# Kernel optimization log

Hardware: AMD Instinct MI355X
Metric: run time of the kernel (lower is better)

Reference implementation:

```python
import jax, jax.numpy as jnp
import numpy as np

NUM_CLASSES = 81
THRESHOLD = 0.5
NEGPOS_RATIO = 3
VARIANCE = (0.1, 0.2)


def point_form(p):
    # center-size -> corner form
    return jnp.concatenate([p[:, :2] - p[:, 2:] / 2, p[:, :2] + p[:, 2:] / 2], axis=1)


def jaccard(box_a, box_b):
    # box_a: [O,4] corners, box_b: [P,4] corners -> IoU [O,P]
    lt = jnp.maximum(box_a[:, None, :2], box_b[None, :, :2])
    rb = jnp.minimum(box_a[:, None, 2:], box_b[None, :, 2:])
    wh = jnp.clip(rb - lt, 0.0)
    inter = wh[..., 0] * wh[..., 1]
    area_a = ((box_a[:, 2] - box_a[:, 0]) * (box_a[:, 3] - box_a[:, 1]))[:, None]
    area_b = ((box_b[:, 2] - box_b[:, 0]) * (box_b[:, 3] - box_b[:, 1]))[None, :]
    return inter / (area_a + area_b - inter)


def encode(matched, priors, variances):
    # matched: [P,4] corner GT, priors: [P,4] center-size
    g_cxcy = (matched[:, :2] + matched[:, 2:]) / 2 - priors[:, :2]
    g_cxcy = g_cxcy / (variances[0] * priors[:, 2:])
    g_wh = (matched[:, 2:] - matched[:, :2]) / priors[:, 2:]
    g_wh = jnp.log(g_wh) / variances[1]
    return jnp.concatenate([g_cxcy, g_wh], axis=1)


def match_one(truths, labels, priors):
    overlaps = jaccard(truths, point_form(priors))   # [O,P]
    best_prior_idx = jnp.argmax(overlaps, axis=1)     # [O] best prior per truth
    best_truth_overlap = jnp.max(overlaps, axis=0)    # [P]
    best_truth_idx = jnp.argmax(overlaps, axis=0)     # [P] best truth per prior
    # force each truth's best prior to match that truth
    best_truth_overlap = best_truth_overlap.at[best_prior_idx].set(2.0)
    best_truth_idx = best_truth_idx.at[best_prior_idx].set(jnp.arange(truths.shape[0]))
    matched = truths[best_truth_idx]                  # [P,4]
    conf = labels[best_truth_idx].astype(jnp.int32) + 1
    conf = jnp.where(best_truth_overlap < THRESHOLD, 0, conf)
    loc = encode(matched, priors, VARIANCE)
    return loc, conf


def _loss(loc_data, conf_data, targets, priors):
    B, P, C = conf_data.shape
    loc_t, conf_t = jax.vmap(lambda t: match_one(t[:, :4], t[:, 4], priors))(targets)
    pos = conf_t > 0                                  # [B,P]
    # smooth-L1 (beta=1) over positive priors, sum reduction
    d = loc_data - loc_t
    sl1 = jnp.where(jnp.abs(d) < 1.0, 0.5 * d * d, jnp.abs(d) - 0.5)
    loss_l = jnp.sum(jnp.where(pos[..., None], sl1, 0.0))
    # per-prior CE used both for mining ranking and the final conf loss
    ce = jax.nn.logsumexp(conf_data, axis=-1) - jnp.take_along_axis(
        conf_data, conf_t[..., None], axis=-1)[..., 0]   # [B,P]
    # hard negative mining: zero positives, double argsort for rank
    loss_c_rank = jnp.where(pos, 0.0, ce)
    loss_idx = jnp.argsort(-loss_c_rank, axis=1)
    idx_rank = jnp.argsort(loss_idx, axis=1)
    num_pos = jnp.sum(pos, axis=1, keepdims=True)     # [B,1]
    num_neg = jnp.minimum(NEGPOS_RATIO * num_pos, P - 1)
    neg = idx_rank < num_neg
    sel = pos | neg
    loss_c = jnp.sum(jnp.where(sel, ce, 0.0))
    N = jnp.sum(num_pos).astype(loc_data.dtype)
    return loss_l / N, loss_c / N


def setup_inputs():
    key = jax.random.key(0)
    kl, kc, kb1, kb2, kll, kp1, kp2 = jax.random.split(key, 7)
    B, P, O, C = 64, 8732, 50, NUM_CLASSES
    loc_data = jax.random.normal(kl, (B, P, 4), jnp.float32)
    conf_data = jax.random.normal(kc, (B, P, C), jnp.float32)
    # valid GT boxes in corner form inside [0,1]
    cxcy = jax.random.uniform(kb1, (B, O, 2), minval=0.2, maxval=0.8)
    wh = jax.random.uniform(kb2, (B, O, 2), minval=0.05, maxval=0.3)
    boxes = jnp.concatenate([cxcy - wh / 2, cxcy + wh / 2], axis=-1)
    labels = jax.random.randint(kll, (B, O), 0, C - 1).astype(jnp.float32)
    targets = jnp.concatenate([boxes, labels[..., None]], axis=-1)  # [B,O,5]
    # priors in center-size form
    pcxcy = jax.random.uniform(kp1, (P, 2), minval=0.05, maxval=0.95)
    pwh = jax.random.uniform(kp2, (P, 2), minval=0.05, maxval=0.5)
    priors = jnp.concatenate([pcxcy, pwh], axis=-1)
    return {"loc_data": loc_data, "conf_data": conf_data, "targets": targets, "priors": priors}


def reference(loc_data, conf_data, targets, priors):
    return _loss(loc_data, conf_data, targets, priors)
```

## Files before the change

### kernel.cpp

```cpp
#include <hip/hip_runtime.h>
#include <float.h>

#pragma clang fp contract(off)

typedef unsigned long long ull;
typedef unsigned int u32;

#define THRESH 0.5f
#define PPT 4
#define CE_R 128
#define SEL_T 512
#define ENC_SEG 1024


__device__ __forceinline__ float sl1(float d) {
    float a = fabsf(d);
    return (a < 1.f) ? 0.5f * d * d : a - 0.5f;
}

__global__ __launch_bounds__(256) void k_match(
        const float* __restrict__ targets, const float* __restrict__ priors,
        float* __restrict__ bto, int* __restrict__ bti, int P, int O, int SEG) {
    const int b = blockIdx.y, seg = blockIdx.x;
    __shared__ float4 tbox[128];
    __shared__ float tarea[128];
    const float* trow = targets + (size_t)b * O * 5;
    for (int o = threadIdx.x; o < O; o += blockDim.x) {
        float x1 = trow[o * 5 + 0], y1 = trow[o * 5 + 1];
        float x2 = trow[o * 5 + 2], y2 = trow[o * 5 + 3];
        tbox[o] = make_float4(x1, y1, x2, y2);
        tarea[o] = (x2 - x1) * (y2 - y1);
    }
    __syncthreads();
    const int p0 = seg * SEG;
    float px1[PPT], py1[PPT], px2[PPT], py2[PPT], pa[PPT];
    float bestv[PPT]; int besto[PPT]; int pidx[PPT];
#pragma unroll
    for (int j = 0; j < PPT; j++) {
        int p = p0 + (int)threadIdx.x + j * 256;
        pidx[j] = p; bestv[j] = -1.f; besto[j] = 0;
        if (p < P) {
            float4 pr = ((const float4*)priors)[p];
            px1[j] = pr.x - pr.z / 2.f;
            py1[j] = pr.y - pr.w / 2.f;
            px2[j] = pr.x + pr.z / 2.f;
            py2[j] = pr.y + pr.w / 2.f;
            pa[j] = (px2[j] - px1[j]) * (py2[j] - py1[j]);
        } else {
            px1[j] = 2.f; py1[j] = 2.f; px2[j] = 2.f; py2[j] = 2.f; pa[j] = 1.f;
        }
    }
    for (int o = 0; o < O; o++) {
        float4 t = tbox[o];
        float ta = tarea[o];
#pragma unroll
        for (int j = 0; j < PPT; j++) {
            float lx = fmaxf(t.x, px1[j]), ly = fmaxf(t.y, py1[j]);
            float rx = fminf(t.z, px2[j]), ry = fminf(t.w, py2[j]);
            float wx = fmaxf(rx - lx, 0.f), wy = fmaxf(ry - ly, 0.f);
            float inter = wx * wy;
            float iou = 0.f;
            if (inter > 0.f) iou = inter / (ta + pa[j] - inter);
            if (iou > bestv[j]) { bestv[j] = iou; besto[j] = o; }
        }
    }
#pragma unroll
    for (int j = 0; j < PPT; j++) {
        if (pidx[j] < P) {
            bto[(size_t)b * P + pidx[j]] = bestv[j];
            bti[(size_t)b * P + pidx[j]] = besto[j];
        }
    }
}

__global__ __launch_bounds__(256) void k_tbest(
        const float* __restrict__ targets, const float* __restrict__ priors,
        ull* __restrict__ tbest, int P, int O, int npairs) {
    int g = blockIdx.x * 4 + ((int)threadIdx.x >> 6);
    int lane = threadIdx.x & 63;
    if (g >= npairs) return;
    int OP = (O + 1) >> 1;
    int b = g / OP;
    int o0 = (g % OP) * 2;
    const float* trow = targets + ((size_t)b * O + o0) * 5;
    float ax1 = trow[0], ay1 = trow[1], ax2 = trow[2], ay2 = trow[3];
    float ta0 = (ax2 - ax1) * (ay2 - ay1);
    bool has1 = (o0 + 1) < O;
    float cx1 = 0, cy1 = 0, cx2 = 0, cy2 = 0, ta1 = 1.f;
    if (has1) {
        cx1 = trow[5]; cy1 = trow[6]; cx2 = trow[7]; cy2 = trow[8];
        ta1 = (cx2 - cx1) * (cy2 - cy1);
    }
    ull k0 = 0, k1 = 0;
    for (int p = lane; p < P; p += 64) {
        float4 pr = ((const float4*)priors)[p];
        float bx1 = pr.x - pr.z / 2.f;
        float by1 = pr.y - pr.w / 2.f;
        float bx2 = pr.x + pr.z / 2.f;
        float by2 = pr.y + pr.w / 2.f;
        float pa = (bx2 - bx1) * (by2 - by1);
        u32 np = ~(u32)p;
        {
            float lx = fmaxf(ax1, bx1), ly = fmaxf(ay1, by1);
            float rx = fminf(ax2, bx2), ry = fminf(ay2, by2);
            float wx = fmaxf(rx - lx, 0.f), wy = fmaxf(ry - ly, 0.f);
            float inter = wx * wy;
            float iou = 0.f;
            if (inter > 0.f) iou = inter / (ta0 + pa - inter);
            ull key = ((ull)__float_as_uint(iou) << 32) | np;
            if (key > k0) k0 = key;
        }
        if (has1) {
            float lx = fmaxf(cx1, bx1), ly = fmaxf(cy1, by1);
            float rx = fminf(cx2, bx2), ry = fminf(cy2, by2);
            float wx = fmaxf(rx - lx, 0.f), wy = fmaxf(ry - ly, 0.f);
            float inter = wx * wy;
            float iou = 0.f;
            if (inter > 0.f) iou = inter / (ta1 + pa - inter);
            ull key = ((ull)__float_as_uint(iou) << 32) | np;
            if (key > k1) k1 = key;
        }
    }
    for (int off = 32; off; off >>= 1) {
        ull a = __shfl_xor(k0, off); if (a > k0) k0 = a;
        ull d = __shfl_xor(k1, off); if (d > k1) k1 = d;
    }
    if (lane == 0) {
        tbest[(size_t)b * O + o0] = k0;
        if (has1) tbest[(size_t)b * O + o0 + 1] = k1;
    }
}

__global__ __launch_bounds__(256) void k_encode(
        const float* __restrict__ targets, const float* __restrict__ priors,
        const float* __restrict__ loc_data, const ull* __restrict__ tbest,
        const float* __restrict__ bto, int* __restrict__ conf_t,
        int* __restrict__ num_pos, float* __restrict__ loss_l,
        int P, int O, int SEG) {
    const int b = blockIdx.y, seg = blockIdx.x;
    __shared__ float tr[64 * 5];
    __shared__ int ov[ENC_SEG];
    __shared__ float redf[4]; __shared__ int redi[4];
    const int p0 = seg * SEG;
    const int p1 = min(p0 + SEG, P);
    const float* trow = targets + (size_t)b * O * 5;
    for (int i = threadIdx.x; i < O * 5; i += blockDim.x) tr[i] = trow[i];
    for (int i = threadIdx.x; i < p1 - p0; i += blockDim.x) ov[i] = -1;
    __syncthreads();
    if ((int)threadIdx.x < O) {
        ull tb = tbest[(size_t)b * O + threadIdx.x];
        u32 p = ~(u32)(tb & 0xFFFFFFFFULL);
        if (p >= (u32)P) p = 0;
        if ((int)p >= p0 && (int)p < p1) atomicMax(&ov[p - p0], (int)threadIdx.x);
    }
    __syncthreads();
    float ll = 0.f; int cnt = 0;
    for (int p = p0 + (int)threadIdx.x; p < p1; p += blockDim.x) {
        size_t idx = (size_t)b * P + p;
        int o = conf_t[idx];
        int ovv = ov[p - p0];
        bool forced = ovv >= 0;
        if (forced) o = ovv;
        float ovl = bto[idx];
        int conf = (!forced && ovl < THRESH) ? 0 : ((int)tr[o * 5 + 4] + 1);
        conf_t[idx] = conf;
        if (conf > 0) {
            cnt++;
            float4 pr = ((const float4*)priors)[p];
            float mx1 = tr[o * 5], my1 = tr[o * 5 + 1];
            float mx2 = tr[o * 5 + 2], my2 = tr[o * 5 + 3];
            float gx = ((mx1 + mx2) / 2.f - pr.x) / (0.1f * pr.z);
            float gy = ((my1 + my2) / 2.f - pr.y) / (0.1f * pr.w);
            float gw = logf((mx2 - mx1) / pr.z) / 0.2f;
            float gh = logf((my2 - my1) / pr.w) / 0.2f;
            float4 ld = ((const float4*)loc_data)[idx];
            ll += sl1(ld.x - gx) + sl1(ld.y - gy) + sl1(ld.z - gw) + sl1(ld.w - gh);
        }
    }
    for (int off = 32; off; off >>= 1) {
        ll += __shfl_down(ll, off);
        cnt += __shfl_down(cnt, off);
    }
    int w = threadIdx.x >> 6;
    if ((threadIdx.x & 63) == 0) { redf[w] = ll; redi[w] = cnt; }
    __syncthreads();
    if (threadIdx.x == 0) {
        float l = 0; int c = 0;
        for (int i = 0; i < 4; i++) { l += redf[i]; c += redi[i]; }
        if (c) atomicAdd(&num_pos[b], c);
        atomicAdd(&loss_l[b], l);
    }
}

__global__ __launch_bounds__(256) void k_ce(
        const float* __restrict__ conf, const int* __restrict__ conf_t,
        float* __restrict__ ce, long long BP) {
    __shared__ float s[CE_R * 81];
    long long r0 = (long long)blockIdx.x * CE_R;
    int nrow = (int)min((long long)CE_R, BP - r0);
    int nfl = nrow * 81;
    const float* src = conf + r0 * 81;
    int nv4 = nfl >> 2;
    const float4* s4 = (const float4*)src;
    for (int i = threadIdx.x; i < nv4; i += 256)
        ((float4*)s)[i] = s4[i];
    for (int i = (nv4 << 2) + (int)threadIdx.x; i < nfl; i += 256)
        s[i] = src[i];
    __syncthreads();
    int row = threadIdx.x >> 1;
    int half = threadIdx.x & 1;
    if (row < nrow) {
        const float* rp = s + row * 81;
        int c0 = half * 41;
        int cn = half ? 40 : 41;
        float sum = 0.f;
        for (int j = 0; j < cn; j++) sum += __expf(rp[c0 + j]);
        sum += __shfl_xor(sum, 1);
        if (half == 0) {
            long long r = r0 + row;
            int t = conf_t[r];
            ce[r] = __logf(sum) - rp[t];
        }
    }
}

__global__ __launch_bounds__(SEL_T) void k_select(
        const float* __restrict__ ce, const int* __restrict__ conf_t,
        const int* __restrict__ num_pos, const float* __restrict__ loss_l,
        float* __restrict__ acc, u32* __restrict__ ticket,
        float* __restrict__ out, int P, int B) {
    extern __shared__ u32 sk[];
    __shared__ u32 whist[SEL_T / 64][16];
    __shared__ u32 hist[16];
    __shared__ float redf[SEL_T / 64]; __shared__ u32 redu[SEL_T / 64];
    __shared__ u32 sh_pval; __shared__ int sh_rem;
    const int b = blockIdx.x;
    const size_t base = (size_t)b * P;
    const int lane = threadIdx.x & 63;
    const int w = threadIdx.x >> 6;
    const int NW = SEL_T / 64;

    float ps = 0.f;
    for (int p = threadIdx.x; p < P; p += SEL_T) {
        int c = conf_t[base + p];
        float v = ce[base + p];
        u32 key;
        if (c > 0) { ps += v; key = 0u; }
        else key = __float_as_uint(fmaxf(v, 0.f));
        sk[p] = key;
    }
    for (int off = 32; off; off >>= 1) ps += __shfl_down(ps, off);
    if (lane == 0) redf[w] = ps;
    __syncthreads();
    float pos_sum = 0.f;
    if (threadIdx.x == 0) {
        for (int i = 0; i < NW; i++) pos_sum += redf[i];
    }

    const int np = num_pos[b];
    const int k = min(3 * np, P - 1);
    u32 pval = 0, pmask = 0; int rem = k;
    if (k > 0) {
        for (int shift = 28; shift >= 0; shift -= 4) {
            __syncthreads();
            ull a0 = 0, a1 = 0;
            for (int p = threadIdx.x; p < P; p += SEL_T) {
                u32 key = sk[p];
                if ((key & pmask) == pval) {
                    u32 dig = (key >> shift) & 15u;
                    ull inc = 1ull << ((dig & 7u) * 8u);
                    if (dig < 8u) a0 += inc; else a1 += inc;
                }
            }
            const ull M = 0x00FF00FF00FF00FFull;
            ull e0 = a0 & M, e1 = (a0 >> 8) & M, e2 = a1 & M, e3 = (a1 >> 8) & M;
            for (int off = 32; off; off >>= 1) {
                e0 += __shfl_xor(e0, off);
                e1 += __shfl_xor(e1, off);
                e2 += __shfl_xor(e2, off);
                e3 += __shfl_xor(e3, off);
            }
            if (lane == 0) {
#pragma unroll
                for (int j = 0; j < 4; j++) {
                    whist[w][2 * j]     = (u32)((e0 >> (16 * j)) & 0xFFFF);
                    whist[w][2 * j + 1] = (u32)((e1 >> (16 * j)) & 0xFFFF);
                    whist[w][8 + 2 * j]     = (u32)((e2 >> (16 * j)) & 0xFFFF);
                    whist[w][8 + 2 * j + 1] = (u32)((e3 >> (16 * j)) & 0xFFFF);
                }
            }
            __syncthreads();
            if (threadIdx.x < 16) {
                u32 h = 0;
                for (int i = 0; i < NW; i++) h += whist[i][threadIdx.x];
                hist[threadIdx.x] = h;
            }
            __syncthreads();
            if (threadIdx.x == 0) {
                u32 accu = 0; int d = 15;
                for (; d > 0; d--) {
                    u32 h = hist[d];
                    if (accu + h >= (u32)rem) break;
                    accu += h;
                }
                sh_pval = pval | ((u32)d << shift);
                sh_rem = rem - (int)accu;
            }
            __syncthreads();
            pval = sh_pval; rem = sh_rem; pmask |= (0xFu << shift);
        }
    }

    float sgt = 0.f; u32 cgt = 0;
    if (k > 0) {
        for (int p = threadIdx.x; p < P; p += SEL_T) {
            u32 key = sk[p];
            if (key > pval) { sgt += __uint_as_float(key); cgt++; }
        }
    }
    for (int off = 32; off; off >>= 1) {
        sgt += __shfl_down(sgt, off);
        cgt += __shfl_down(cgt, off);
    }
    __syncthreads();
    if (lane == 0) { redf[w] = sgt; redu[w] = cgt; }
    __syncthreads();
    if (threadIdx.x == 0) {
        float s = 0.f; u32 c = 0;
        for (int i = 0; i < NW; i++) { s += redf[i]; c += redu[i]; }
        float t = __uint_as_float(pval);
        float lc_b = pos_sum + ((k > 0) ? (s + (float)(k - (int)c) * t) : 0.f);
        atomicAdd(&acc[0], (float)np);
        atomicAdd(&acc[1], loss_l[b]);
        atomicAdd(&acc[2], lc_b);
        __threadfence();
        u32 tk = atomicAdd(ticket, 1u);
        if (tk == (u32)(B - 1)) {
            float n  = atomicAdd(&acc[0], 0.f);
            float ll = atomicAdd(&acc[1], 0.f);
            float lc = atomicAdd(&acc[2], 0.f);
            out[0] = ll / n;
            out[1] = lc / n;
        }
    }
}


extern "C" void kernel_launch(void* const* d_in, const int* in_sizes, int n_in,
                              void* d_out, int out_size, void* d_ws, size_t ws_size,
                              hipStream_t stream) {
    const float* loc     = (const float*)d_in[0];
    const float* conf    = (const float*)d_in[1];
    const float* targets = (const float*)d_in[2];
    const float* priors  = (const float*)d_in[3];

    const int P = in_sizes[3] / 4;
    const int B = in_sizes[0] / (P * 4);
    const int O = in_sizes[2] / (B * 5);

    char* ws = (char*)d_ws;
    size_t off = 0;
    int*   num_pos = (int*)(ws + off);   off += (size_t)B * sizeof(int);
    float* loss_l  = (float*)(ws + off); off += (size_t)B * sizeof(float);
    float* acc     = (float*)(ws + off); off += 4 * sizeof(float);
    u32*   ticket  = (u32*)(ws + off);   off += sizeof(u32);
    const size_t zbytes = off;
    off = (off + 7) & ~(size_t)7;
    ull*   tbest   = (ull*)(ws + off);   off += (size_t)B * O * sizeof(ull);
    float* F       = (float*)(ws + off); off += (size_t)B * P * sizeof(float);
    int*   I       = (int*)(ws + off);   off += (size_t)B * P * sizeof(int);

    (void)hipMemsetAsync(d_ws, 0, zbytes, stream);

    const int SEG = 256 * PPT;
    const int S = (P + SEG - 1) / SEG;
    k_match<<<dim3(S, B), 256, 0, stream>>>(targets, priors, F, I, P, O, SEG);

    const int npairs = B * ((O + 1) / 2);
    k_tbest<<<(npairs + 3) / 4, 256, 0, stream>>>(targets, priors, tbest, P, O, npairs);

    const int S2 = (P + ENC_SEG - 1) / ENC_SEG;
    const int SEG2 = (P + S2 - 1) / S2;
    k_encode<<<dim3(S2, B), 256, 0, stream>>>(targets, priors, loc, tbest, F, I,
                                              num_pos, loss_l, P, O, SEG2);

    const long long BP = (long long)B * P;
    k_ce<<<(int)((BP + CE_R - 1) / CE_R), 256, 0, stream>>>(conf, I, F, BP);

    k_select<<<B, SEL_T, (size_t)P * sizeof(u32), stream>>>(F, I, num_pos, loss_l,
                                                            acc, ticket, (float*)d_out, P, B);
}
```

Baseline: 404.9 us.

## Fuse per-truth best-prior search into match and merge encode into CE kernel

The per-truth best-prior argmax is now computed inside k_match through shared-memory and global atomicMax, which removes the separate k_tbest pass over priors. The encode/localization-loss work and the negative key construction move into the cross-entropy kernel, so conf_t is never materialised and k_select no longer makes a second pass to build keys and positive sums. This cuts two launches and several full B*P reads and writes. In exchange it adds atomic contention on tbest and per-block handling of two batches per tile.

```diff
diff --git a/kernel.cpp b/kernel.cpp
--- a/kernel.cpp
+++ b/kernel.cpp
@@ -10,7 +10,6 @@
 #define PPT 4
 #define CE_R 128
 #define SEL_T 512
-#define ENC_SEG 1024
 
 
 __device__ __forceinline__ float sl1(float d) {
@@ -20,16 +19,19 @@
 
 __global__ __launch_bounds__(256) void k_match(
         const float* __restrict__ targets, const float* __restrict__ priors,
-        float* __restrict__ bto, int* __restrict__ bti, int P, int O, int SEG) {
+        float* __restrict__ bto, int* __restrict__ bti,
+        ull* __restrict__ tbest, int P, int O, int SEG) {
     const int b = blockIdx.y, seg = blockIdx.x;
-    __shared__ float4 tbox[128];
-    __shared__ float tarea[128];
+    __shared__ float4 tbox[64];
+    __shared__ float tarea[64];
+    __shared__ ull bestL[64];
     const float* trow = targets + (size_t)b * O * 5;
     for (int o = threadIdx.x; o < O; o += blockDim.x) {
         float x1 = trow[o * 5 + 0], y1 = trow[o * 5 + 1];
         float x2 = trow[o * 5 + 2], y2 = trow[o * 5 + 3];
         tbox[o] = make_float4(x1, y1, x2, y2);
         tarea[o] = (x2 - x1) * (y2 - y1);
+        bestL[o] = 0ull;
     }
     __syncthreads();
     const int p0 = seg * SEG;
@@ -53,6 +55,7 @@
     for (int o = 0; o < O; o++) {
         float4 t = tbox[o];
         float ta = tarea[o];
+        float vmax = -1.f; int pmax = 0;
 #pragma unroll
         for (int j = 0; j < PPT; j++) {
             float lx = fmaxf(t.x, px1[j]), ly = fmaxf(t.y, py1[j]);
@@ -62,8 +65,13 @@
             float iou = 0.f;
             if (inter > 0.f) iou = inter / (ta + pa[j] - inter);
             if (iou > bestv[j]) { bestv[j] = iou; besto[j] = o; }
-        }
-    }
+            if (iou > vmax) { vmax = iou; pmax = pidx[j]; }
+        }
+        ull key = ((ull)__float_as_uint(vmax) << 32) | (u32)(~(u32)pmax);
+        ull cur = bestL[o];
+        if (key > cur) atomicMax(&bestL[o], key);
+    }
+    __syncthreads();
 #pragma unroll
     for (int j = 0; j < PPT; j++) {
         if (pidx[j] < P) {
@@ -71,144 +79,57 @@
             bti[(size_t)b * P + pidx[j]] = besto[j];
         }
     }
-}
-
-__global__ __launch_bounds__(256) void k_tbest(
-        const float* __restrict__ targets, const float* __restrict__ priors,
-        ull* __restrict__ tbest, int P, int O, int npairs) {
-    int g = blockIdx.x * 4 + ((int)threadIdx.x >> 6);
-    int lane = threadIdx.x & 63;
-    if (g >= npairs) return;
-    int OP = (O + 1) >> 1;
-    int b = g / OP;
-    int o0 = (g % OP) * 2;
-    const float* trow = targets + ((size_t)b * O + o0) * 5;
-    float ax1 = trow[0], ay1 = trow[1], ax2 = trow[2], ay2 = trow[3];
-    float ta0 = (ax2 - ax1) * (ay2 - ay1);
-    bool has1 = (o0 + 1) < O;
-    float cx1 = 0, cy1 = 0, cx2 = 0, cy2 = 0, ta1 = 1.f;
-    if (has1) {
-        cx1 = trow[5]; cy1 = trow[6]; cx2 = trow[7]; cy2 = trow[8];
-        ta1 = (cx2 - cx1) * (cy2 - cy1);
-    }
-    ull k0 = 0, k1 = 0;
-    for (int p = lane; p < P; p += 64) {
-        float4 pr = ((const float4*)priors)[p];
-        float bx1 = pr.x - pr.z / 2.f;
-        float by1 = pr.y - pr.w / 2.f;
-        float bx2 = pr.x + pr.z / 2.f;
-        float by2 = pr.y + pr.w / 2.f;
-        float pa = (bx2 - bx1) * (by2 - by1);
-        u32 np = ~(u32)p;
-        {
-            float lx = fmaxf(ax1, bx1), ly = fmaxf(ay1, by1);
-            float rx = fminf(ax2, bx2), ry = fminf(ay2, by2);
-            float wx = fmaxf(rx - lx, 0.f), wy = fmaxf(ry - ly, 0.f);
-            float inter = wx * wy;
-            float iou = 0.f;
-            if (inter > 0.f) iou = inter / (ta0 + pa - inter);
-            ull key = ((ull)__float_as_uint(iou) << 32) | np;
-            if (key > k0) k0 = key;
-        }
-        if (has1) {
-            float lx = fmaxf(cx1, bx1), ly = fmaxf(cy1, by1);
-            float rx = fminf(cx2, bx2), ry = fminf(cy2, by2);
-            float wx = fmaxf(rx - lx, 0.f), wy = fmaxf(ry - ly, 0.f);
-            float inter = wx * wy;
-            float iou = 0.f;
-            if (inter > 0.f) iou = inter / (ta1 + pa - inter);
-            ull key = ((ull)__float_as_uint(iou) << 32) | np;
-            if (key > k1) k1 = key;
-        }
-    }
-    for (int off = 32; off; off >>= 1) {
-        ull a = __shfl_xor(k0, off); if (a > k0) k0 = a;
-        ull d = __shfl_xor(k1, off); if (d > k1) k1 = d;
-    }
-    if (lane == 0) {
-        tbest[(size_t)b * O + o0] = k0;
-        if (has1) tbest[(size_t)b * O + o0 + 1] = k1;
-    }
-}
-
-__global__ __launch_bounds__(256) void k_encode(
-        const float* __restrict__ targets, const float* __restrict__ priors,
-        const float* __restrict__ loc_data, const ull* __restrict__ tbest,
-        const float* __restrict__ bto, int* __restrict__ conf_t,
+    for (int o = threadIdx.x; o < O; o += blockDim.x)
+        atomicMax(&tbest[(size_t)b * O + o], bestL[o]);
+}
+
+__global__ __launch_bounds__(256) void k_fused(
+        const float* __restrict__ conf, const float* __restrict__ targets,
+        const float* __restrict__ priors, const float* __restrict__ loc_data,
+        const ull* __restrict__ tbest, const float* __restrict__ bto,
+        int* bti_keys,
         int* __restrict__ num_pos, float* __restrict__ loss_l,
-        int P, int O, int SEG) {
-    const int b = blockIdx.y, seg = blockIdx.x;
-    __shared__ float tr[64 * 5];
-    __shared__ int ov[ENC_SEG];
-    __shared__ float redf[4]; __shared__ int redi[4];
-    const int p0 = seg * SEG;
-    const int p1 = min(p0 + SEG, P);
-    const float* trow = targets + (size_t)b * O * 5;
-    for (int i = threadIdx.x; i < O * 5; i += blockDim.x) tr[i] = trow[i];
-    for (int i = threadIdx.x; i < p1 - p0; i += blockDim.x) ov[i] = -1;
-    __syncthreads();
-    if ((int)threadIdx.x < O) {
-        ull tb = tbest[(size_t)b * O + threadIdx.x];
-        u32 p = ~(u32)(tb & 0xFFFFFFFFULL);
-        if (p >= (u32)P) p = 0;
-        if ((int)p >= p0 && (int)p < p1) atomicMax(&ov[p - p0], (int)threadIdx.x);
-    }
-    __syncthreads();
-    float ll = 0.f; int cnt = 0;
-    for (int p = p0 + (int)threadIdx.x; p < p1; p += blockDim.x) {
-        size_t idx = (size_t)b * P + p;
-        int o = conf_t[idx];
-        int ovv = ov[p - p0];
-        bool forced = ovv >= 0;
-        if (forced) o = ovv;
-        float ovl = bto[idx];
-        int conf = (!forced && ovl < THRESH) ? 0 : ((int)tr[o * 5 + 4] + 1);
-        conf_t[idx] = conf;
-        if (conf > 0) {
-            cnt++;
-            float4 pr = ((const float4*)priors)[p];
-            float mx1 = tr[o * 5], my1 = tr[o * 5 + 1];
-            float mx2 = tr[o * 5 + 2], my2 = tr[o * 5 + 3];
-            float gx = ((mx1 + mx2) / 2.f - pr.x) / (0.1f * pr.z);
-            float gy = ((my1 + my2) / 2.f - pr.y) / (0.1f * pr.w);
-            float gw = logf((mx2 - mx1) / pr.z) / 0.2f;
-            float gh = logf((my2 - my1) / pr.w) / 0.2f;
-            float4 ld = ((const float4*)loc_data)[idx];
-            ll += sl1(ld.x - gx) + sl1(ld.y - gy) + sl1(ld.z - gw) + sl1(ld.w - gh);
-        }
-    }
-    for (int off = 32; off; off >>= 1) {
-        ll += __shfl_down(ll, off);
-        cnt += __shfl_down(cnt, off);
-    }
-    int w = threadIdx.x >> 6;
-    if ((threadIdx.x & 63) == 0) { redf[w] = ll; redi[w] = cnt; }
-    __syncthreads();
-    if (threadIdx.x == 0) {
-        float l = 0; int c = 0;
-        for (int i = 0; i < 4; i++) { l += redf[i]; c += redi[i]; }
-        if (c) atomicAdd(&num_pos[b], c);
-        atomicAdd(&loss_l[b], l);
-    }
-}
-
-__global__ __launch_bounds__(256) void k_ce(
-        const float* __restrict__ conf, const int* __restrict__ conf_t,
-        float* __restrict__ ce, long long BP) {
+        float* __restrict__ lcpos, int P, int O, long long BP) {
     __shared__ float s[CE_R * 81];
-    long long r0 = (long long)blockIdx.x * CE_R;
-    int nrow = (int)min((long long)CE_R, BP - r0);
+    __shared__ float tr[2][64 * 5];
+    __shared__ int ov[CE_R];
+    __shared__ float redf[4]; __shared__ int redi[4]; __shared__ float redp[4];
+    const long long r0 = (long long)blockIdx.x * CE_R;
+    const int nrow = (int)min((long long)CE_R, BP - r0);
+
     int nfl = nrow * 81;
     const float* src = conf + r0 * 81;
     int nv4 = nfl >> 2;
-    const float4* s4 = (const float4*)src;
     for (int i = threadIdx.x; i < nv4; i += 256)
-        ((float4*)s)[i] = s4[i];
+        ((float4*)s)[i] = ((const float4*)src)[i];
     for (int i = (nv4 << 2) + (int)threadIdx.x; i < nfl; i += 256)
         s[i] = src[i];
-    __syncthreads();
-    int row = threadIdx.x >> 1;
-    int half = threadIdx.x & 1;
+
+    const int b0 = (int)(r0 / P);
+    const int b1 = (int)((r0 + nrow - 1) / P);
+    const int nb = (b1 != b0) ? 2 : 1;
+    for (int i = threadIdx.x; i < O * 5; i += 256)
+        tr[0][i] = targets[(size_t)b0 * O * 5 + i];
+    if (nb == 2)
+        for (int i = threadIdx.x; i < O * 5; i += 256)
+            tr[1][i] = targets[(size_t)b1 * O * 5 + i];
+    if ((int)threadIdx.x < CE_R) ov[threadIdx.x] = -1;
+    __syncthreads();
+
+    for (int i = threadIdx.x; i < nb * O; i += 256) {
+        int which = i / O, o = i - which * O;
+        int bx = which ? b1 : b0;
+        ull tb = tbest[(size_t)bx * O + o];
+        u32 p = ~(u32)(tb & 0xFFFFFFFFull);
+        if (p >= (u32)P) p = 0;
+        long long r = (long long)bx * P + p;
+        if (r >= r0 && r < r0 + nrow) atomicMax(&ov[(int)(r - r0)], o);
+    }
+    __syncthreads();
+
+    const int row = threadIdx.x >> 1;
+    const int half = threadIdx.x & 1;
+    float ll = 0.f, ps = 0.f; int cnt = 0, myb = -1;
     if (row < nrow) {
         const float* rp = s + row * 81;
         int c0 = half * 41;
@@ -218,15 +139,63 @@
         sum += __shfl_xor(sum, 1);
         if (half == 0) {
             long long r = r0 + row;
-            int t = conf_t[r];
-            ce[r] = __logf(sum) - rp[t];
-        }
+            int b = (int)(r / P); myb = b;
+            int p = (int)(r - (long long)b * P);
+            const float* trb = tr[(b == b0) ? 0 : 1];
+            int o = bti_keys[r];
+            int ovv = ov[row];
+            bool forced = ovv >= 0;
+            if (forced) o = ovv;
+            float ovl = bto[r];
+            int cf = (!forced && ovl < THRESH) ? 0 : ((int)trb[o * 5 + 4] + 1);
+            float ce = __logf(sum) - rp[cf];
+            u32 key;
+            if (cf > 0) {
+                cnt = 1; ps = ce; key = 0u;
+                float4 pr = ((const float4*)priors)[p];
+                float mx1 = trb[o * 5], my1 = trb[o * 5 + 1];
+                float mx2 = trb[o * 5 + 2], my2 = trb[o * 5 + 3];
+                float gx = ((mx1 + mx2) / 2.f - pr.x) / (0.1f * pr.z);
+                float gy = ((my1 + my2) / 2.f - pr.y) / (0.1f * pr.w);
+                float gw = logf((mx2 - mx1) / pr.z) / 0.2f;
+                float gh = logf((my2 - my1) / pr.w) / 0.2f;
+                float4 ld = ((const float4*)loc_data)[r];
+                ll = sl1(ld.x - gx) + sl1(ld.y - gy) + sl1(ld.z - gw) + sl1(ld.w - gh);
+            } else {
+                key = __float_as_uint(fmaxf(ce, 0.f));
+            }
+            ((u32*)bti_keys)[r] = key;
+        }
+    }
+    const int w = threadIdx.x >> 6;
+    for (int pass = 0; pass < nb; pass++) {
+        int bx = pass ? b1 : b0;
+        float llv = (myb == bx) ? ll : 0.f;
+        float pv  = (myb == bx) ? ps : 0.f;
+        int   cv  = (myb == bx) ? cnt : 0;
+        for (int off = 32; off; off >>= 1) {
+            llv += __shfl_down(llv, off);
+            pv  += __shfl_down(pv, off);
+            cv  += __shfl_down(cv, off);
+        }
+        if ((threadIdx.x & 63) == 0) { redf[w] = llv; redp[w] = pv; redi[w] = cv; }
+        __syncthreads();
+        if (threadIdx.x == 0) {
+            float l = 0.f, q = 0.f; int c = 0;
+            for (int i = 0; i < 4; i++) { l += redf[i]; q += redp[i]; c += redi[i]; }
+            if (c) {
+                atomicAdd(&num_pos[bx], c);
+                atomicAdd(&loss_l[bx], l);
+                atomicAdd(&lcpos[bx], q);
+            }
+        }
+        __syncthreads();
     }
 }
 
 __global__ __launch_bounds__(SEL_T) void k_select(
-        const float* __restrict__ ce, const int* __restrict__ conf_t,
-        const int* __restrict__ num_pos, const float* __restrict__ loss_l,
+        const u32* __restrict__ keys, const int* __restrict__ num_pos,
+        const float* __restrict__ loss_l, const float* __restrict__ lcpos,
         float* __restrict__ acc, u32* __restrict__ ticket,
         float* __restrict__ out, int P, int B) {
     extern __shared__ u32 sk[];
@@ -240,22 +209,7 @@
     const int w = threadIdx.x >> 6;
     const int NW = SEL_T / 64;
 
-    float ps = 0.f;
-    for (int p = threadIdx.x; p < P; p += SEL_T) {
-        int c = conf_t[base + p];
-        float v = ce[base + p];
-        u32 key;
-        if (c > 0) { ps += v; key = 0u; }
-        else key = __float_as_uint(fmaxf(v, 0.f));
-        sk[p] = key;
-    }
-    for (int off = 32; off; off >>= 1) ps += __shfl_down(ps, off);
-    if (lane == 0) redf[w] = ps;
-    __syncthreads();
-    float pos_sum = 0.f;
-    if (threadIdx.x == 0) {
-        for (int i = 0; i < NW; i++) pos_sum += redf[i];
-    }
+    for (int p = threadIdx.x; p < P; p += SEL_T) sk[p] = keys[base + p];
 
     const int np = num_pos[b];
     const int k = min(3 * np, P - 1);
@@ -283,8 +237,8 @@
             if (lane == 0) {
 #pragma unroll
                 for (int j = 0; j < 4; j++) {
-                    whist[w][2 * j]     = (u32)((e0 >> (16 * j)) & 0xFFFF);
-                    whist[w][2 * j + 1] = (u32)((e1 >> (16 * j)) & 0xFFFF);
+                    whist[w][2 * j]         = (u32)((e0 >> (16 * j)) & 0xFFFF);
+                    whist[w][2 * j + 1]     = (u32)((e1 >> (16 * j)) & 0xFFFF);
                     whist[w][8 + 2 * j]     = (u32)((e2 >> (16 * j)) & 0xFFFF);
                     whist[w][8 + 2 * j + 1] = (u32)((e3 >> (16 * j)) & 0xFFFF);
                 }
@@ -329,7 +283,7 @@
         float s = 0.f; u32 c = 0;
         for (int i = 0; i < NW; i++) { s += redf[i]; c += redu[i]; }
         float t = __uint_as_float(pval);
-        float lc_b = pos_sum + ((k > 0) ? (s + (float)(k - (int)c) * t) : 0.f);
+        float lc_b = lcpos[b] + ((k > 0) ? (s + (float)(k - (int)c) * t) : 0.f);
         atomicAdd(&acc[0], (float)np);
         atomicAdd(&acc[1], loss_l[b]);
         atomicAdd(&acc[2], lc_b);
@@ -360,13 +314,14 @@
 
     char* ws = (char*)d_ws;
     size_t off = 0;
+    ull*   tbest   = (ull*)(ws + off);   off += (size_t)B * O * sizeof(ull);
     int*   num_pos = (int*)(ws + off);   off += (size_t)B * sizeof(int);
     float* loss_l  = (float*)(ws + off); off += (size_t)B * sizeof(float);
+    float* lcpos   = (float*)(ws + off); off += (size_t)B * sizeof(float);
     float* acc     = (float*)(ws + off); off += 4 * sizeof(float);
     u32*   ticket  = (u32*)(ws + off);   off += sizeof(u32);
     const size_t zbytes = off;
-    off = (off + 7) & ~(size_t)7;
-    ull*   tbest   = (ull*)(ws + off);   off += (size_t)B * O * sizeof(ull);
+    off = (off + 15) & ~(size_t)15;
     float* F       = (float*)(ws + off); off += (size_t)B * P * sizeof(float);
     int*   I       = (int*)(ws + off);   off += (size_t)B * P * sizeof(int);
 
@@ -374,19 +329,12 @@
 
     const int SEG = 256 * PPT;
     const int S = (P + SEG - 1) / SEG;
-    k_match<<<dim3(S, B), 256, 0, stream>>>(targets, priors, F, I, P, O, SEG);
-
-    const int npairs = B * ((O + 1) / 2);
-    k_tbest<<<(npairs + 3) / 4, 256, 0, stream>>>(targets, priors, tbest, P, O, npairs);
-
-    const int S2 = (P + ENC_SEG - 1) / ENC_SEG;
-    const int SEG2 = (P + S2 - 1) / S2;
-    k_encode<<<dim3(S2, B), 256, 0, stream>>>(targets, priors, loc, tbest, F, I,
-                                              num_pos, loss_l, P, O, SEG2);
+    k_match<<<dim3(S, B), 256, 0, stream>>>(targets, priors, F, I, tbest, P, O, SEG);
 
     const long long BP = (long long)B * P;
-    k_ce<<<(int)((BP + CE_R - 1) / CE_R), 256, 0, stream>>>(conf, I, F, BP);
-
-    k_select<<<B, SEL_T, (size_t)P * sizeof(u32), stream>>>(F, I, num_pos, loss_l,
-                                                            acc, ticket, (float*)d_out, P, B);
-}
+    k_fused<<<(int)((BP + CE_R - 1) / CE_R), 256, 0, stream>>>(
+        conf, targets, priors, loc, tbest, F, I, num_pos, loss_l, lcpos, P, O, BP);
+
+    k_select<<<B, SEL_T, (size_t)P * sizeof(u32), stream>>>(
+        (const u32*)I, num_pos, loss_l, lcpos, acc, ticket, (float*)d_out, P, B);
+}
```

New measurement: 557.3 us. +37.7%, slower.
